# Performance work log

Measured on AMD Instinct MI355X. Metric: run time of the kernel, lower is better.

The kernel has to match this reference:

```python
import jax, jax.numpy as jnp
import numpy as np

N_BONDS = 16777216
N_ATOMS = 1048576
N_TYPES = 16


def setup_inputs() -> dict:
    key = jax.random.key(0)
    k1, k2, k3, k4, k5, k6 = jax.random.split(key, 6)
    # bond orders kept strictly positive so BO**p_be2 and its grad are finite
    bo_sigma = jax.random.uniform(k1, (N_BONDS,), jnp.float32, 0.05, 1.0)
    bo_pi = jax.random.uniform(k2, (N_BONDS,), jnp.float32, 0.05, 1.0)
    bo_pipi = jax.random.uniform(k3, (N_BONDS,), jnp.float32, 0.05, 1.0)
    bond_type = jax.random.randint(k4, (N_BONDS,), 0, N_TYPES, jnp.int32)
    atom_i = jax.random.randint(k5, (N_BONDS,), 0, N_ATOMS, jnp.int32)
    # columns: De_sigma, De_pi, De_pipi, p_be1, p_be2 (positive, O(1))
    bond_params = jax.random.uniform(k6, (N_TYPES, 5), jnp.float32, 0.1, 1.0)
    return {
        "bond_type": bond_type,
        "atom_i": atom_i,
        "bo_sigma": bo_sigma,
        "bo_pi": bo_pi,
        "bo_pipi": bo_pipi,
        "bond_params": bond_params,
        "n_atoms": N_ATOMS,
    }


def reference(bond_type, atom_i, bo_sigma, bo_pi, bo_pipi, bond_params, n_atoms):
    # Gather per-bond-type parameters: [E, 5]
    p = bond_params[bond_type]
    de_s, de_p, de_pp, p_be1, p_be2 = (p[:, 0], p[:, 1], p[:, 2], p[:, 3], p[:, 4])
    # ReaxFF bond energy per bond
    e_bond = (-de_s * bo_sigma * jnp.exp(p_be1 * (1.0 - bo_sigma ** p_be2))
              - de_p * bo_pi
              - de_pp * bo_pipi)
    # Scatter-reduce to per-atom energy
    e_atom = jax.ops.segment_sum(e_bond, atom_i, num_segments=n_atoms)
    return e_atom
```

## Files before the change

kernel.cpp:

```cpp
#include <hip/hip_runtime.h>


typedef float    f32x4 __attribute__((ext_vector_type(4)));
typedef int      i32x4 __attribute__((ext_vector_type(4)));
typedef unsigned u32x4 __attribute__((ext_vector_type(4)));
typedef unsigned u32;
typedef unsigned short u16;

#define NBUK   64
#define RANGEK 16384
#define SHIFTK 14
#define CB     8192
#define TB     256
#define PADQ   16u
#define SPLITS 4

__device__ __forceinline__ u32 f32_to_bf16_bits(float f) {
    u32 u = __float_as_uint(f);
    return ((u + 0x7FFFu + ((u >> 16) & 1u)) >> 16) & 0xFFFFu;
}

__global__ __launch_bounds__(TB) void count_kernel(
        const i32x4* __restrict__ atom_i, u16* __restrict__ counts,
        int round_start) {
    __shared__ u32 hist[4][NBUK];
    int tid = threadIdx.x, w = tid >> 6;
    if (tid < 4 * NBUK) ((u32*)hist)[tid] = 0u;
    __syncthreads();
    long base4 = ((long)round_start + (long)blockIdx.x * CB) >> 2;
#pragma unroll
    for (int it = 0; it < CB / (TB * 4); ++it) {
        i32x4 a = __builtin_nontemporal_load(&atom_i[base4 + it * TB + tid]);
        atomicAdd(&hist[w][(u32)a.x >> SHIFTK], 1u);
        atomicAdd(&hist[w][(u32)a.y >> SHIFTK], 1u);
        atomicAdd(&hist[w][(u32)a.z >> SHIFTK], 1u);
        atomicAdd(&hist[w][(u32)a.w >> SHIFTK], 1u);
    }
    __syncthreads();
    if (tid < NBUK)
        counts[(size_t)blockIdx.x * NBUK + tid] =
            (u16)(hist[0][tid] + hist[1][tid] + hist[2][tid] + hist[3][tid]);
}

__global__ __launch_bounds__(TB) void scan_cols_kernel(
        const u16* __restrict__ counts, u32* __restrict__ offs,
        u32* __restrict__ total, int nsb) {
    __shared__ u32 sc[TB];
    int b = blockIdx.x, t = threadIdx.x;
    int vpt = nsb >> 8;
    u32 v[8];
    u32 s = 0;
    for (int k = 0; k < vpt; ++k) {
        u32 c = counts[(size_t)(t * vpt + k) * NBUK + b];
        c = (c + PADQ - 1u) & ~(PADQ - 1u);
        v[k] = s; s += c;
    }
    sc[t] = s;
    __syncthreads();
    for (int off = 1; off < TB; off <<= 1) {
        u32 u = (t >= off) ? sc[t - off] : 0u;
        __syncthreads();
        sc[t] += u;
        __syncthreads();
    }
    u32 excl = sc[t] - s;
    for (int k = 0; k < vpt; ++k)
        offs[(size_t)(t * vpt + k) * NBUK + b] = excl + v[k];
    if (t == TB - 1) total[b] = sc[t];
}

__global__ __launch_bounds__(64) void base_kernel(
        const u32* __restrict__ total, u32* __restrict__ gbase) {
    int t = threadIdx.x;
    u32 v = total[t];
    u32 s = v;
#pragma unroll
    for (int off = 1; off < 64; off <<= 1) {
        u32 n = __shfl_up(s, off);
        if (t >= off) s += n;
    }
    gbase[t] = s - v;
}

__global__ __launch_bounds__(TB, 4) void partition_kernel(
        const i32x4* __restrict__ bt, const i32x4* __restrict__ ai,
        const f32x4* __restrict__ bs_, const f32x4* __restrict__ bp_,
        const f32x4* __restrict__ bpp_, const float* __restrict__ bond_params,
        const u16* __restrict__ counts, const u32* __restrict__ offs,
        const u32* __restrict__ gbase, u32* __restrict__ arena,
        int round_start) {
    __shared__ u32   sorted[CB];
    __shared__ u32   start_[NBUK], cur[NBUK], gofs[NBUK];
    __shared__ float4 sp_a[16];
    __shared__ float  sp_b[16];

    int tid = threadIdx.x, sb = blockIdx.x;
    if (tid < 16) {
        const float* p = bond_params + tid * 5;
        sp_a[tid] = make_float4(p[0], p[1], p[2], p[3]);
        sp_b[tid] = p[4];
    }
    if (tid < 64) {
        u32 c = counts[(size_t)sb * NBUK + tid];
        u32 s = c;
#pragma unroll
        for (int off = 1; off < 64; off <<= 1) {
            u32 n = __shfl_up(s, off);
            if (tid >= off) s += n;
        }
        u32 excl = s - c;
        start_[tid] = excl;
        cur[tid]    = excl;
        gofs[tid]   = gbase[tid] + offs[(size_t)sb * NBUK + tid];
    }
    __syncthreads();

    long base4 = ((long)round_start + (long)sb * CB) >> 2;
#pragma unroll
    for (int it = 0; it < CB / (TB * 4); ++it) {
        long idx = base4 + it * TB + tid;
        i32x4 t  = __builtin_nontemporal_load(&bt[idx]);
        i32x4 a  = __builtin_nontemporal_load(&ai[idx]);
        f32x4 s  = __builtin_nontemporal_load(&bs_[idx]);
        f32x4 p  = __builtin_nontemporal_load(&bp_[idx]);
        f32x4 pp = __builtin_nontemporal_load(&bpp_[idx]);
#pragma unroll
        for (int k = 0; k < 4; ++k) {
            u32 ak = (u32)a[k];
            float4 pa = sp_a[t[k]];
            float  pb = sp_b[t[k]];
            float pw = __powf(s[k], pb);
            float e  = -pa.x * s[k] * __expf(pa.w * (1.0f - pw))
                       - pa.y * p[k] - pa.z * pp[k];
            u32 b = ak >> SHIFTK;
            u32 pos = atomicAdd(&cur[b], 1u);
            sorted[pos] = ((ak & (RANGEK - 1u)) << 16) | f32_to_bf16_bits(e);
        }
    }
    __syncthreads();

    int w = tid >> 6, lane = tid & 63;
    for (int b = w; b < NBUK; b += 4) {
        u32 end = cur[b], ls = start_[b], len = end - ls;
        u32 plen = (len + PADQ - 1u) & ~(PADQ - 1u);
        u32 g = gofs[b];
        for (u32 j = lane; j < plen; j += 64u)
            arena[g + j] = (j < len) ? sorted[ls + j] : 0u;
    }
}

__global__ __launch_bounds__(1024) void accum_kernel(
        const u32* __restrict__ arena, const u32* __restrict__ total,
        const u32* __restrict__ gbase, float* __restrict__ partials) {
    __shared__ float acc[RANGEK];
    int tid = threadIdx.x;
    int b = blockIdx.x >> 2, sp = blockIdx.x & 3;
    f32x4* a4 = (f32x4*)acc;
#pragma unroll
    for (int i = 0; i < RANGEK / 4 / 1024; ++i)
        a4[i * 1024 + tid] = (f32x4)(0.f);
    __syncthreads();
    u32 s0 = gbase[b];
    u32 n  = total[b];
    u32 qs = n >> 4;
    const u32x4* src = (const u32x4*)(arena + s0) + (size_t)sp * qs;
    for (u32 j = tid; j < qs; j += 1024) {
        u32x4 e = __builtin_nontemporal_load(&src[j]);
        atomicAdd(&acc[e.x >> 16], __uint_as_float((e.x & 0xFFFFu) << 16));
        atomicAdd(&acc[e.y >> 16], __uint_as_float((e.y & 0xFFFFu) << 16));
        atomicAdd(&acc[e.z >> 16], __uint_as_float((e.z & 0xFFFFu) << 16));
        atomicAdd(&acc[e.w >> 16], __uint_as_float((e.w & 0xFFFFu) << 16));
    }
    __syncthreads();
    f32x4* pr = (f32x4*)(partials + ((size_t)sp * NBUK + b) * RANGEK);
#pragma unroll
    for (int i = 0; i < RANGEK / 4 / 1024; ++i)
        pr[i * 1024 + tid] = a4[i * 1024 + tid];
}

__global__ __launch_bounds__(TB) void merge_kernel(
        const float* __restrict__ partials, float* __restrict__ out,
        int n_atoms, int add_prev) {
    int i = blockIdx.x * TB + threadIdx.x;
    const f32x4* p0 = (const f32x4*)partials;
    const f32x4* p1 = (const f32x4*)(partials + (size_t)n_atoms);
    const f32x4* p2 = (const f32x4*)(partials + 2 * (size_t)n_atoms);
    const f32x4* p3 = (const f32x4*)(partials + 3 * (size_t)n_atoms);
    f32x4* o4 = (f32x4*)out;
    f32x4 v = p0[i] + p1[i] + p2[i] + p3[i];
    if (add_prev) v += o4[i];
    o4[i] = v;
}

__global__ __launch_bounds__(TB) void zero_kernel(f32x4* __restrict__ p, int n4) {
    int i = blockIdx.x * blockDim.x + threadIdx.x;
    if (i < n4) p[i] = (f32x4)(0.f);
}

__global__ __launch_bounds__(TB) void atomic_fallback_kernel(
        const i32x4* __restrict__ bt, const i32x4* __restrict__ ai,
        const f32x4* __restrict__ bs_, const f32x4* __restrict__ bp_,
        const f32x4* __restrict__ bpp_, const float* __restrict__ bond_params,
        float* __restrict__ out, int n4) {
    __shared__ float sp[80];
    if (threadIdx.x < 80) sp[threadIdx.x] = bond_params[threadIdx.x];
    __syncthreads();
    int i = blockIdx.x * blockDim.x + threadIdx.x;
    if (i >= n4) return;
    i32x4 t  = bt[i]; i32x4 a = ai[i];
    f32x4 s  = bs_[i]; f32x4 p = bp_[i]; f32x4 pp = bpp_[i];
#pragma unroll
    for (int k = 0; k < 4; ++k) {
        const float* pr = sp + t[k] * 5;
        float pw = __powf(s[k], pr[4]);
        float e  = -pr[0] * s[k] * __expf(pr[3] * (1.0f - pw))
                   - pr[1] * p[k] - pr[2] * pp[k];
        unsafeAtomicAdd(&out[a[k]], e);
    }
}

extern "C" void kernel_launch(void* const* d_in, const int* in_sizes, int n_in,
                              void* d_out, int out_size, void* d_ws, size_t ws_size,
                              hipStream_t stream) {
    const int*   bond_type   = (const int*)  d_in[0];
    const int*   atom_i      = (const int*)  d_in[1];
    const float* bo_sigma    = (const float*)d_in[2];
    const float* bo_pi       = (const float*)d_in[3];
    const float* bo_pipi     = (const float*)d_in[4];
    const float* bond_params = (const float*)d_in[5];
    float*       e_atom      = (float*)d_out;

    const int n_bonds = in_sizes[0];
    const int n_atoms = out_size;

    int cfg_nr = 0;
    if (n_atoms == (NBUK << SHIFTK)) {
        const int cands[5] = {1, 2, 4, 8, 16};
        for (int ci = 0; ci < 5 && !cfg_nr; ++ci) {
            int r = cands[ci];
            if (n_bonds % (r * CB)) continue;
            long cpr = (long)n_bonds / r, nsb = cpr / CB;
            if (nsb % 256 || nsb < 256 || nsb > 4096) continue;
            size_t arena_worst = (size_t)cpr + (size_t)(PADQ - 1) * NBUK * nsb;
            size_t need = arena_worst * 4
                        + (size_t)nsb * NBUK * 4
                        + (size_t)NBUK * 8
                        + (size_t)nsb * NBUK * 2
                        + (size_t)SPLITS * n_atoms * 4
                        + 256;
            if (need <= ws_size) cfg_nr = r;
        }
    }

    if (cfg_nr) {
        const int NR = cfg_nr, cpr = n_bonds / NR, nsb = cpr / CB;
        size_t arena_worst = (size_t)cpr + (size_t)(PADQ - 1) * NBUK * nsb;
        u32*   arena    = (u32*)d_ws;
        u32*   offs     = arena + arena_worst;
        u32*   total    = offs + (size_t)nsb * NBUK;
        u32*   gbase    = total + NBUK;
        u16*   counts   = (u16*)(gbase + NBUK);
        float* partials = (float*)(counts + (size_t)nsb * NBUK);
        for (int r = 0; r < NR; ++r) {
            int rs = r * cpr;
            count_kernel<<<nsb, TB, 0, stream>>>((const i32x4*)atom_i, counts, rs);
            scan_cols_kernel<<<NBUK, TB, 0, stream>>>(counts, offs, total, nsb);
            base_kernel<<<1, 64, 0, stream>>>(total, gbase);
            partition_kernel<<<nsb, TB, 0, stream>>>(
                (const i32x4*)bond_type, (const i32x4*)atom_i,
                (const f32x4*)bo_sigma, (const f32x4*)bo_pi, (const f32x4*)bo_pipi,
                bond_params, counts, offs, gbase, arena, rs);
            accum_kernel<<<NBUK * SPLITS, 1024, 0, stream>>>(
                arena, total, gbase, partials);
            merge_kernel<<<n_atoms / 4 / TB, TB, 0, stream>>>(
                partials, e_atom, n_atoms, r ? 1 : 0);
        }
    } else {
        int zn4 = n_atoms / 4;
        zero_kernel<<<(zn4 + TB - 1) / TB, TB, 0, stream>>>((f32x4*)e_atom, zn4);
        int n4 = n_bonds / 4;
        atomic_fallback_kernel<<<(n4 + TB - 1) / TB, TB, 0, stream>>>(
            (const i32x4*)bond_type, (const i32x4*)atom_i,
            (const f32x4*)bo_sigma, (const f32x4*)bo_pi, (const f32x4*)bo_pipi,
            bond_params, e_atom, n4);
    }
}
```

Measured before the change: 423.6 us.

## Fuse counting into partition kernel and allocate bucket slabs with global atomics

Removes the separate count, column-scan and base kernels. Each partition block now builds its bucket histogram in shared memory and reserves space in a per-bucket fixed-size slab through a global atomicAdd cursor. Overflowing buckets fall back to direct atomics into the output. This saves a full extra read of atom_i and several launches, at the cost of contention on the global cursors, non-deterministic ordering, and a fixed slab footprint. Padding is reduced to 8, and the accum kernel's splits now interleave strided over each slab.

Result: slower. 437.8 us (+3.3%).

```diff
diff --git a/kernel.cpp b/kernel.cpp
--- a/kernel.cpp
+++ b/kernel.cpp
@@ -5,125 +5,79 @@
 typedef int      i32x4 __attribute__((ext_vector_type(4)));
 typedef unsigned u32x4 __attribute__((ext_vector_type(4)));
 typedef unsigned u32;
-typedef unsigned short u16;
 
 #define NBUK   64
 #define RANGEK 16384
 #define SHIFTK 14
 #define CB     8192
 #define TB     256
-#define PADQ   16u
+#define PADQ   8u
 #define SPLITS 4
 
 __device__ __forceinline__ u32 f32_to_bf16_bits(float f) {
     u32 u = __float_as_uint(f);
     return ((u + 0x7FFFu + ((u >> 16) & 1u)) >> 16) & 0xFFFFu;
-}
-
-__global__ __launch_bounds__(TB) void count_kernel(
-        const i32x4* __restrict__ atom_i, u16* __restrict__ counts,
-        int round_start) {
-    __shared__ u32 hist[4][NBUK];
-    int tid = threadIdx.x, w = tid >> 6;
-    if (tid < 4 * NBUK) ((u32*)hist)[tid] = 0u;
-    __syncthreads();
-    long base4 = ((long)round_start + (long)blockIdx.x * CB) >> 2;
-#pragma unroll
-    for (int it = 0; it < CB / (TB * 4); ++it) {
-        i32x4 a = __builtin_nontemporal_load(&atom_i[base4 + it * TB + tid]);
-        atomicAdd(&hist[w][(u32)a.x >> SHIFTK], 1u);
-        atomicAdd(&hist[w][(u32)a.y >> SHIFTK], 1u);
-        atomicAdd(&hist[w][(u32)a.z >> SHIFTK], 1u);
-        atomicAdd(&hist[w][(u32)a.w >> SHIFTK], 1u);
-    }
-    __syncthreads();
-    if (tid < NBUK)
-        counts[(size_t)blockIdx.x * NBUK + tid] =
-            (u16)(hist[0][tid] + hist[1][tid] + hist[2][tid] + hist[3][tid]);
-}
-
-__global__ __launch_bounds__(TB) void scan_cols_kernel(
-        const u16* __restrict__ counts, u32* __restrict__ offs,
-        u32* __restrict__ total, int nsb) {
-    __shared__ u32 sc[TB];
-    int b = blockIdx.x, t = threadIdx.x;
-    int vpt = nsb >> 8;
-    u32 v[8];
-    u32 s = 0;
-    for (int k = 0; k < vpt; ++k) {
-        u32 c = counts[(size_t)(t * vpt + k) * NBUK + b];
-        c = (c + PADQ - 1u) & ~(PADQ - 1u);
-        v[k] = s; s += c;
-    }
-    sc[t] = s;
-    __syncthreads();
-    for (int off = 1; off < TB; off <<= 1) {
-        u32 u = (t >= off) ? sc[t - off] : 0u;
-        __syncthreads();
-        sc[t] += u;
-        __syncthreads();
-    }
-    u32 excl = sc[t] - s;
-    for (int k = 0; k < vpt; ++k)
-        offs[(size_t)(t * vpt + k) * NBUK + b] = excl + v[k];
-    if (t == TB - 1) total[b] = sc[t];
-}
-
-__global__ __launch_bounds__(64) void base_kernel(
-        const u32* __restrict__ total, u32* __restrict__ gbase) {
-    int t = threadIdx.x;
-    u32 v = total[t];
-    u32 s = v;
-#pragma unroll
-    for (int off = 1; off < 64; off <<= 1) {
-        u32 n = __shfl_up(s, off);
-        if (t >= off) s += n;
-    }
-    gbase[t] = s - v;
 }
 
 __global__ __launch_bounds__(TB, 4) void partition_kernel(
         const i32x4* __restrict__ bt, const i32x4* __restrict__ ai,
         const f32x4* __restrict__ bs_, const f32x4* __restrict__ bp_,
         const f32x4* __restrict__ bpp_, const float* __restrict__ bond_params,
-        const u16* __restrict__ counts, const u32* __restrict__ offs,
-        const u32* __restrict__ gbase, u32* __restrict__ arena,
-        int round_start) {
+        u32* __restrict__ gcur, u32* __restrict__ arena,
+        float* __restrict__ out, u32 slab, int round_start) {
     __shared__ u32   sorted[CB];
-    __shared__ u32   start_[NBUK], cur[NBUK], gofs[NBUK];
+    __shared__ u32   hist[4][NBUK];
+    __shared__ u32   start_[NBUK], cur[NBUK], graw_[NBUK], ovf_[NBUK];
     __shared__ float4 sp_a[16];
     __shared__ float  sp_b[16];
 
     int tid = threadIdx.x, sb = blockIdx.x;
+    ((u32*)hist)[tid] = 0u;
     if (tid < 16) {
         const float* p = bond_params + tid * 5;
         sp_a[tid] = make_float4(p[0], p[1], p[2], p[3]);
         sp_b[tid] = p[4];
     }
+    __syncthreads();
+
+    long base4 = ((long)round_start + (long)sb * CB) >> 2;
+    int w = tid >> 6;
+    i32x4 av[CB / (TB * 4)];
+#pragma unroll
+    for (int it = 0; it < CB / (TB * 4); ++it) {
+        av[it] = ai[base4 + it * TB + tid];
+        atomicAdd(&hist[w][(u32)av[it].x >> SHIFTK], 1u);
+        atomicAdd(&hist[w][(u32)av[it].y >> SHIFTK], 1u);
+        atomicAdd(&hist[w][(u32)av[it].z >> SHIFTK], 1u);
+        atomicAdd(&hist[w][(u32)av[it].w >> SHIFTK], 1u);
+    }
+    __syncthreads();
+
     if (tid < 64) {
-        u32 c = counts[(size_t)sb * NBUK + tid];
+        u32 c = hist[0][tid] + hist[1][tid] + hist[2][tid] + hist[3][tid];
         u32 s = c;
 #pragma unroll
         for (int off = 1; off < 64; off <<= 1) {
             u32 n = __shfl_up(s, off);
             if (tid >= off) s += n;
         }
-        u32 excl = s - c;
-        start_[tid] = excl;
-        cur[tid]    = excl;
-        gofs[tid]   = gbase[tid] + offs[(size_t)sb * NBUK + tid];
-    }
-    __syncthreads();
-
-    long base4 = ((long)round_start + (long)sb * CB) >> 2;
+        start_[tid] = s - c;
+        cur[tid]    = s - c;
+        u32 plen = (c + PADQ - 1u) & ~(PADQ - 1u);
+        u32 g = atomicAdd(&gcur[tid], plen);
+        graw_[tid] = g;
+        ovf_[tid]  = (g + plen > slab) ? 1u : 0u;
+    }
+    __syncthreads();
+
 #pragma unroll
     for (int it = 0; it < CB / (TB * 4); ++it) {
         long idx = base4 + it * TB + tid;
-        i32x4 t  = __builtin_nontemporal_load(&bt[idx]);
-        i32x4 a  = __builtin_nontemporal_load(&ai[idx]);
-        f32x4 s  = __builtin_nontemporal_load(&bs_[idx]);
-        f32x4 p  = __builtin_nontemporal_load(&bp_[idx]);
-        f32x4 pp = __builtin_nontemporal_load(&bpp_[idx]);
+        i32x4 t  = bt[idx];
+        f32x4 s  = bs_[idx];
+        f32x4 p  = bp_[idx];
+        f32x4 pp = bpp_[idx];
+        i32x4 a  = av[it];
 #pragma unroll
         for (int k = 0; k < 4; ++k) {
             u32 ak = (u32)a[k];
@@ -139,19 +93,32 @@
     }
     __syncthreads();
 
-    int w = tid >> 6, lane = tid & 63;
+    int lane = tid & 63;
     for (int b = w; b < NBUK; b += 4) {
-        u32 end = cur[b], ls = start_[b], len = end - ls;
+        u32 ls = start_[b], len = cur[b] - ls;
         u32 plen = (len + PADQ - 1u) & ~(PADQ - 1u);
-        u32 g = gofs[b];
-        for (u32 j = lane; j < plen; j += 64u)
-            arena[g + j] = (j < len) ? sorted[ls + j] : 0u;
+        u32 g = graw_[b];
+        if (!ovf_[b]) {
+            size_t base = (size_t)b * slab + g;
+            for (u32 j = lane; j < plen; j += 64u)
+                arena[base + j] = (j < len) ? sorted[ls + j] : 0u;
+        } else {
+            u32 z0 = g < slab ? g : slab;
+            u32 z1 = (g + plen) < slab ? (g + plen) : slab;
+            for (u32 j = z0 + lane; j < z1; j += 64u)
+                arena[(size_t)b * slab + j] = 0u;
+            for (u32 j = lane; j < len; j += 64u) {
+                u32 e = sorted[ls + j];
+                unsafeAtomicAdd(&out[((u32)b << SHIFTK) + (e >> 16)],
+                                __uint_as_float((e & 0xFFFFu) << 16));
+            }
+        }
     }
 }
 
 __global__ __launch_bounds__(1024) void accum_kernel(
-        const u32* __restrict__ arena, const u32* __restrict__ total,
-        const u32* __restrict__ gbase, float* __restrict__ partials) {
+        const u32* __restrict__ arena, const u32* __restrict__ gcur,
+        float* __restrict__ partials, u32 slab) {
     __shared__ float acc[RANGEK];
     int tid = threadIdx.x;
     int b = blockIdx.x >> 2, sp = blockIdx.x & 3;
@@ -160,11 +127,11 @@
     for (int i = 0; i < RANGEK / 4 / 1024; ++i)
         a4[i * 1024 + tid] = (f32x4)(0.f);
     __syncthreads();
-    u32 s0 = gbase[b];
-    u32 n  = total[b];
-    u32 qs = n >> 4;
-    const u32x4* src = (const u32x4*)(arena + s0) + (size_t)sp * qs;
-    for (u32 j = tid; j < qs; j += 1024) {
+    u32 n = gcur[b];
+    if (n > slab) n = slab;
+    u32 nv = n >> 2;
+    const u32x4* src = (const u32x4*)(arena + (size_t)b * slab);
+    for (u32 j = (u32)sp * 1024u + tid; j < nv; j += 4096u) {
         u32x4 e = __builtin_nontemporal_load(&src[j]);
         atomicAdd(&acc[e.x >> 16], __uint_as_float((e.x & 0xFFFFu) << 16));
         atomicAdd(&acc[e.y >> 16], __uint_as_float((e.y & 0xFFFFu) << 16));
@@ -180,16 +147,14 @@
 
 __global__ __launch_bounds__(TB) void merge_kernel(
         const float* __restrict__ partials, float* __restrict__ out,
-        int n_atoms, int add_prev) {
+        int n_atoms) {
     int i = blockIdx.x * TB + threadIdx.x;
     const f32x4* p0 = (const f32x4*)partials;
     const f32x4* p1 = (const f32x4*)(partials + (size_t)n_atoms);
     const f32x4* p2 = (const f32x4*)(partials + 2 * (size_t)n_atoms);
     const f32x4* p3 = (const f32x4*)(partials + 3 * (size_t)n_atoms);
     f32x4* o4 = (f32x4*)out;
-    f32x4 v = p0[i] + p1[i] + p2[i] + p3[i];
-    if (add_prev) v += o4[i];
-    o4[i] = v;
+    o4[i] += p0[i] + p1[i] + p2[i] + p3[i];
 }
 
 __global__ __launch_bounds__(TB) void zero_kernel(f32x4* __restrict__ p, int n4) {
@@ -233,47 +198,40 @@
     const int n_bonds = in_sizes[0];
     const int n_atoms = out_size;
 
-    int cfg_nr = 0;
+    int cfg_nr = 0; u32 cfg_slab = 0;
     if (n_atoms == (NBUK << SHIFTK)) {
         const int cands[5] = {1, 2, 4, 8, 16};
         for (int ci = 0; ci < 5 && !cfg_nr; ++ci) {
             int r = cands[ci];
             if (n_bonds % (r * CB)) continue;
             long cpr = (long)n_bonds / r, nsb = cpr / CB;
-            if (nsb % 256 || nsb < 256 || nsb > 4096) continue;
-            size_t arena_worst = (size_t)cpr + (size_t)(PADQ - 1) * NBUK * nsb;
-            size_t need = arena_worst * 4
-                        + (size_t)nsb * NBUK * 4
-                        + (size_t)NBUK * 8
-                        + (size_t)nsb * NBUK * 2
-                        + (size_t)SPLITS * n_atoms * 4
-                        + 256;
-            if (need <= ws_size) cfg_nr = r;
+            if (nsb < 256 || nsb > 8192) continue;
+            u32 sl = (u32)((cpr / NBUK + nsb * 4 + 8192 + 7) & ~7L);
+            size_t need = (size_t)NBUK * sl * 4
+                        + 1024
+                        + (size_t)SPLITS * n_atoms * 4;
+            if (need <= ws_size) { cfg_nr = r; cfg_slab = sl; }
         }
     }
 
     if (cfg_nr) {
         const int NR = cfg_nr, cpr = n_bonds / NR, nsb = cpr / CB;
-        size_t arena_worst = (size_t)cpr + (size_t)(PADQ - 1) * NBUK * nsb;
         u32*   arena    = (u32*)d_ws;
-        u32*   offs     = arena + arena_worst;
-        u32*   total    = offs + (size_t)nsb * NBUK;
-        u32*   gbase    = total + NBUK;
-        u16*   counts   = (u16*)(gbase + NBUK);
-        float* partials = (float*)(counts + (size_t)nsb * NBUK);
+        u32*   gcur     = arena + (size_t)NBUK * cfg_slab;
+        float* partials = (float*)(gcur + 256);
+        int zn4 = n_atoms / 4;
+        zero_kernel<<<(zn4 + TB - 1) / TB, TB, 0, stream>>>((f32x4*)e_atom, zn4);
         for (int r = 0; r < NR; ++r) {
             int rs = r * cpr;
-            count_kernel<<<nsb, TB, 0, stream>>>((const i32x4*)atom_i, counts, rs);
-            scan_cols_kernel<<<NBUK, TB, 0, stream>>>(counts, offs, total, nsb);
-            base_kernel<<<1, 64, 0, stream>>>(total, gbase);
+            hipMemsetAsync(gcur, 0, NBUK * sizeof(u32), stream);
             partition_kernel<<<nsb, TB, 0, stream>>>(
                 (const i32x4*)bond_type, (const i32x4*)atom_i,
                 (const f32x4*)bo_sigma, (const f32x4*)bo_pi, (const f32x4*)bo_pipi,
-                bond_params, counts, offs, gbase, arena, rs);
+                bond_params, gcur, arena, e_atom, cfg_slab, rs);
             accum_kernel<<<NBUK * SPLITS, 1024, 0, stream>>>(
-                arena, total, gbase, partials);
+                arena, gcur, partials, cfg_slab);
             merge_kernel<<<n_atoms / 4 / TB, TB, 0, stream>>>(
-                partials, e_atom, n_atoms, r ? 1 : 0);
+                partials, e_atom, n_atoms);
         }
     } else {
         int zn4 = n_atoms / 4;
```
